# Performance work log

Measured on AMD Instinct MI355X. Metric: run time of the kernel, lower is better.

Reference implementation:

```python
import jax, jax.numpy as jnp
import numpy as np

D_MODEL = 1024
D_HEAD = 64
M_BITS = 32


def setup_inputs() -> dict:
    key = jax.random.key(0)
    ks = jax.random.split(key, 6)
    B, N, M = 2, 2048, 2048
    Q = jax.random.normal(ks[0], (B, N, D_MODEL), dtype=jnp.float32)
    K = jax.random.normal(ks[1], (B, M, D_MODEL), dtype=jnp.float32)
    V = jax.random.normal(ks[2], (B, M, D_MODEL), dtype=jnp.float32)
    s = 1.0 / np.sqrt(D_MODEL)
    Wq = jax.random.normal(ks[3], (D_MODEL, M_BITS), dtype=jnp.float32) * s
    Wk = jax.random.normal(ks[4], (D_MODEL, M_BITS), dtype=jnp.float32) * s
    Wv = jax.random.normal(ks[5], (D_MODEL, D_HEAD), dtype=jnp.float32) * s
    temperature = jnp.ones((1,), dtype=jnp.float32)
    return {"Q": Q, "K": K, "V": V, "Wq": Wq, "Wk": Wk, "Wv": Wv,
            "temperature": temperature}


def tropical_matmul(A, Bt):
    # A: [B, N, m], Bt: [B, M, m] (already transposed form of [B, m, M])
    # (A \odot B)_{ij} = min_k (A_ik + B_kj)
    return jnp.min(A[:, :, None, :] + Bt[:, None, :, :], axis=-1)  # [B, N, M]


def reference(Q, K, V, Wq, Wk, Wv, temperature):
    # REWA tropical encoders (continuous): linear projections to m_bits
    Qt = jnp.einsum('bnd,dm->bnm', Q, Wq)   # [B, N, m_bits]
    Kt = jnp.einsum('bsd,dm->bsm', K, Wk)   # [B, M, m_bits]
    Vp = jnp.einsum('bsd,dh->bsh', V, Wv)   # [B, M, d_head]
    # tropical (min-plus) scores, negated so shorter paths score higher
    scores = -tropical_matmul(Qt, Kt)       # [B, N, M]
    scores = scores / jax.nn.softplus(temperature[0])
    attn = jax.nn.softmax(scores, axis=-1)  # [B, N, M]
    out = jnp.einsum('bnm,bmh->bnh', attn, Vp)  # [B, N, d_head]
    return out, attn
```

## Files before the change

### kernel.cpp

```cpp
#include <hip/hip_runtime.h>
#include <math.h>

#define DM 1024
#define NB 2048
#define MBITS 32
#define DH 64

typedef __attribute__((ext_vector_type(4))) float floatx4;
typedef __attribute__((ext_vector_type(8))) short shortx8;

__device__ __forceinline__ unsigned short f32_to_bf16(float f) {
    union { float f; unsigned u; } v; v.f = f;
    unsigned r = v.u + 0x7FFF + ((v.u >> 16) & 1);
    return (unsigned short)(r >> 16);
}

__device__ __forceinline__ void split2(float x0, float x1, unsigned& hp, unsigned& lp) {
    union { float f; unsigned u; } a, b; a.f = x0; b.f = x1;
    unsigned h0 = a.u & 0xFFFF0000u, h1 = b.u & 0xFFFF0000u;
    union { unsigned u; float f; } hf0, hf1; hf0.u = h0; hf1.u = h1;
    union { float f; unsigned u; } c, d;
    c.f = x0 - hf0.f;
    d.f = x1 - hf1.f;
    hp = (h0 >> 16) | h1;
    lp = (c.u >> 16) | (d.u & 0xFFFF0000u);
}

__global__ __launch_bounds__(256) void wprep_kernel(
    const float* __restrict__ Wq, const float* __restrict__ Wk,
    const float* __restrict__ Wv, unsigned short* __restrict__ Wf)
{
    int wv = blockIdx.x * 4 + (threadIdx.x >> 6);
    int l  = threadIdx.x & 63;
    const float* W; int C, kc32, ct;
    if (wv < 64)       { W = Wq; C = 32; kc32 = wv >> 1;  ct = wv & 1; }
    else if (wv < 128) { W = Wk; C = 32; int z = wv - 64;  kc32 = z >> 1; ct = z & 1; }
    else               { W = Wv; C = 64; int z = wv - 128; kc32 = z >> 2; ct = z & 3; }
    int k0 = kc32 * 32 + (l >> 4) * 8;
    int c  = ct * 16 + (l & 15);
    float x[8];
    #pragma unroll
    for (int j = 0; j < 8; ++j) x[j] = W[(size_t)(k0 + j) * C + c];
    unsigned hp[4], lp[4];
    #pragma unroll
    for (int j2 = 0; j2 < 4; ++j2) split2(x[2 * j2], x[2 * j2 + 1], hp[j2], lp[j2]);
    uint4 hv; hv.x = hp[0]; hv.y = hp[1]; hv.z = hp[2]; hv.w = hp[3];
    uint4 lv; lv.x = lp[0]; lv.y = lp[1]; lv.z = lp[2]; lv.w = lp[3];
    *(uint4*)&Wf[(size_t)wv * 1024 + l * 8]       = hv;
    *(uint4*)&Wf[(size_t)wv * 1024 + 512 + l * 8] = lv;
}

__global__ __launch_bounds__(512) void proj_mfma2_kernel(
    const float* __restrict__ Q, const float* __restrict__ K, const float* __restrict__ V,
    const unsigned short* __restrict__ Wf,
    float* __restrict__ Qt, float* __restrict__ KtT, unsigned short* __restrict__ VpT)
{
    __shared__ float red[8][64][16];

    int gb = blockIdx.x;
    int job = gb >> 8, tile = gb & 255;
    int r0 = tile * 16;
    const float* X = (job == 0) ? Q : (job == 1) ? K : V;
    int ntct  = (job == 2) ? 4 : 2;
    int pbase = job << 6;
    int t = threadIdx.x, w = t >> 6, l = t & 63;
    int lrow = l & 15, lq = l >> 4;

    const float* xrow = &X[(size_t)(r0 + lrow) * DM + w * 128 + lq * 8];

    floatx4 acc[4];
    #pragma unroll
    for (int i = 0; i < 4; ++i) acc[i] = (floatx4){0.f, 0.f, 0.f, 0.f};

    #pragma unroll
    for (int s = 0; s < 4; ++s) {
        floatx4 g0 = *(const floatx4*)(xrow + s * 32);
        floatx4 g1 = *(const floatx4*)(xrow + s * 32 + 4);
        union { unsigned u[4]; shortx8 v; } ahi, alo;
        split2(g0.x, g0.y, ahi.u[0], alo.u[0]);
        split2(g0.z, g0.w, ahi.u[1], alo.u[1]);
        split2(g1.x, g1.y, ahi.u[2], alo.u[2]);
        split2(g1.z, g1.w, ahi.u[3], alo.u[3]);
        int kc32 = w * 4 + s;
        #pragma unroll
        for (int ct = 0; ct < 4; ++ct) {
            if (ct >= ntct) break;
            int p = pbase + kc32 * ntct + ct;
            const unsigned short* wp = &Wf[(size_t)p * 1024 + l * 8];
            shortx8 bhi = *(const shortx8*)wp;
            shortx8 blo = *(const shortx8*)(wp + 512);
            acc[ct] = __builtin_amdgcn_mfma_f32_16x16x32_bf16(ahi.v, bhi, acc[ct], 0, 0, 0);
            acc[ct] = __builtin_amdgcn_mfma_f32_16x16x32_bf16(ahi.v, blo, acc[ct], 0, 0, 0);
            acc[ct] = __builtin_amdgcn_mfma_f32_16x16x32_bf16(alo.v, bhi, acc[ct], 0, 0, 0);
        }
    }

    #pragma unroll
    for (int ct = 0; ct < 4; ++ct) {
        if (ct >= ntct) break;
        #pragma unroll
        for (int r = 0; r < 4; ++r) red[w][l][ct * 4 + r] = acc[ct][r];
    }
    __syncthreads();

    int r = w & 3, ct0 = w >> 2;
    int row = r0 + lq * 4 + r;
    if (job == 0) {
        float v = red[0][l][ct0 * 4 + r] + red[1][l][ct0 * 4 + r]
                + red[2][l][ct0 * 4 + r] + red[3][l][ct0 * 4 + r]
                + red[4][l][ct0 * 4 + r] + red[5][l][ct0 * 4 + r]
                + red[6][l][ct0 * 4 + r] + red[7][l][ct0 * 4 + r];
        Qt[(size_t)row * MBITS + ct0 * 16 + lrow] = v;
    } else if (job == 1) {
        int bb = row >> 11, j = row & 2047;
        float v = red[0][l][ct0 * 4 + r] + red[1][l][ct0 * 4 + r]
                + red[2][l][ct0 * 4 + r] + red[3][l][ct0 * 4 + r]
                + red[4][l][ct0 * 4 + r] + red[5][l][ct0 * 4 + r]
                + red[6][l][ct0 * 4 + r] + red[7][l][ct0 * 4 + r];
        KtT[(size_t)bb * (MBITS * NB) + (size_t)(ct0 * 16 + lrow) * NB + j] = v;
    } else {
        int bb = row >> 11, j = row & 2047;
        #pragma unroll
        for (int cti = 0; cti < 2; ++cti) {
            int ct = ct0 + 2 * cti;
            float v = red[0][l][ct * 4 + r] + red[1][l][ct * 4 + r]
                    + red[2][l][ct * 4 + r] + red[3][l][ct * 4 + r]
                    + red[4][l][ct * 4 + r] + red[5][l][ct * 4 + r]
                    + red[6][l][ct * 4 + r] + red[7][l][ct * 4 + r];
            VpT[(size_t)bb * (DH * NB) + (size_t)(ct * 16 + lrow) * NB + j] = f32_to_bf16(v);
        }
    }
}

__global__ __attribute__((amdgpu_waves_per_eu(4, 4))) __launch_bounds__(1024)
void fused_score_out_kernel(
    const float* __restrict__ Qt, const float* __restrict__ KtT,
    const unsigned short* __restrict__ VpT, const float* __restrict__ temp,
    float* __restrict__ outp, float* __restrict__ attn)
{
    __shared__ unsigned short Elds[16][2056];
    __shared__ float redsum2[16][2];

    const int b  = blockIdx.y;
    const int i0 = blockIdx.x * 16;
    const int t  = threadIdx.x;
    const int w  = t >> 6, l = t & 63;

    const float tv = temp[0];
    const float c2 = -(1.0f / log1pf(__expf(tv))) * 1.44269504088896340736f;

    {
        const int ip  = w & 7;
        const int jhb = (w >> 3) * 1024;
        const int p   = l >> 4;
        const int l16 = l & 15;

        const float* Qbase = &Qt[(size_t)(b * NB + i0 + ip * 2) * MBITS + p * 8];
        floatx4 qa0 = *(const floatx4*)(Qbase);
        floatx4 qa1 = *(const floatx4*)(Qbase + 4);
        floatx4 qb0 = *(const floatx4*)(Qbase + MBITS);
        floatx4 qb1 = *(const floatx4*)(Qbase + MBITS + 4);

        const float* Kp = &KtT[(size_t)b * (MBITS * NB) + (size_t)(p * 8) * NB];
        float sacc0 = 0.f, sacc1 = 0.f;

        #pragma unroll 1
        for (int s = 0; s < 8; ++s) {
            const int j0 = jhb + s * 128 + l16 * 8;
            float m0[8], m1[8];
            #pragma unroll
            for (int jj = 0; jj < 8; ++jj) { m0[jj] = 1e30f; m1[jj] = 1e30f; }

            #pragma unroll
            for (int kp = 0; kp < 8; ++kp) {
                const float* kr = Kp + (size_t)kp * NB + j0;
                floatx4 k0 = *(const floatx4*)kr;
                floatx4 k1 = *(const floatx4*)(kr + 4);
                float qa = (kp < 4) ? qa0[kp] : qa1[kp - 4];
                float qb = (kp < 4) ? qb0[kp] : qb1[kp - 4];
                float kv[8] = {k0.x, k0.y, k0.z, k0.w, k1.x, k1.y, k1.z, k1.w};
                #pragma unroll
                for (int jj = 0; jj < 8; ++jj) {
                    m0[jj] = fminf(m0[jj], qa + kv[jj]);
                    m1[jj] = fminf(m1[jj], qb + kv[jj]);
                }
            }
            #pragma unroll
            for (int jj = 0; jj < 8; ++jj) {
                m0[jj] = fminf(m0[jj], __shfl_xor(m0[jj], 16, 64));
                m0[jj] = fminf(m0[jj], __shfl_xor(m0[jj], 32, 64));
                m1[jj] = fminf(m1[jj], __shfl_xor(m1[jj], 16, 64));
                m1[jj] = fminf(m1[jj], __shfl_xor(m1[jj], 32, 64));
            }
            float e0[8], e1[8];
            #pragma unroll
            for (int jj = 0; jj < 8; ++jj) {
                e0[jj] = exp2f(c2 * m0[jj]);
                e1[jj] = exp2f(c2 * m1[jj]);
            }
            uint4 u0, u1;
            u0.x = (unsigned)f32_to_bf16(e0[0]) | ((unsigned)f32_to_bf16(e0[1]) << 16);
            u0.y = (unsigned)f32_to_bf16(e0[2]) | ((unsigned)f32_to_bf16(e0[3]) << 16);
            u0.z = (unsigned)f32_to_bf16(e0[4]) | ((unsigned)f32_to_bf16(e0[5]) << 16);
            u0.w = (unsigned)f32_to_bf16(e0[6]) | ((unsigned)f32_to_bf16(e0[7]) << 16);
            u1.x = (unsigned)f32_to_bf16(e1[0]) | ((unsigned)f32_to_bf16(e1[1]) << 16);
            u1.y = (unsigned)f32_to_bf16(e1[2]) | ((unsigned)f32_to_bf16(e1[3]) << 16);
            u1.z = (unsigned)f32_to_bf16(e1[4]) | ((unsigned)f32_to_bf16(e1[5]) << 16);
            u1.w = (unsigned)f32_to_bf16(e1[6]) | ((unsigned)f32_to_bf16(e1[7]) << 16);
            if (l < 16) {
                *(uint4*)&Elds[ip * 2][j0]     = u0;
                *(uint4*)&Elds[ip * 2 + 1][j0] = u1;
            }
            float s0 = ((e0[0] + e0[1]) + (e0[2] + e0[3])) + ((e0[4] + e0[5]) + (e0[6] + e0[7]));
            float s1 = ((e1[0] + e1[1]) + (e1[2] + e1[3])) + ((e1[4] + e1[5]) + (e1[6] + e1[7]));
            #pragma unroll
            for (int off = 1; off < 16; off <<= 1) {
                s0 += __shfl_xor(s0, off, 64);
                s1 += __shfl_xor(s1, off, 64);
            }
            sacc0 += s0; sacc1 += s1;
        }
        if (l == 0) { redsum2[w][0] = sacc0; redsum2[w][1] = sacc1; }
    }
    __syncthreads();

    const int mrow = l & 15, q4 = l >> 4;
    const int hh  = (w & 3) * 16 + mrow;
    const int kg  = w >> 2;
    floatx4 acc = {0.f, 0.f, 0.f, 0.f};
    const unsigned short* Vb = &VpT[(size_t)b * (DH * NB) + (size_t)hh * NB];

    #pragma unroll
    for (int jc2 = 0; jc2 < 8; ++jc2) {
        #pragma unroll
        for (int t2 = 0; t2 < 2; ++t2) {
            int ks = kg * 2 + t2;
            int joff = jc2 * 256 + ks * 32 + q4 * 8;
            shortx8 a  = *(const shortx8*)&Elds[mrow][joff];
            shortx8 bf = *(const shortx8*)&Vb[joff];
            acc = __builtin_amdgcn_mfma_f32_16x16x32_bf16(a, bf, acc, 0, 0, 0);
        }
    }

    {
        float iv = 1.0f / (redsum2[w >> 1][w & 1] + redsum2[8 + (w >> 1)][w & 1]);
        #pragma unroll
        for (int u = 0; u < 8; ++u) {
            int j = u * 256 + l * 4;
            uint2 pk = *(const uint2*)&Elds[w][j];
            union { unsigned u; float f; } x0, x1, x2, x3;
            x0.u = pk.x << 16; x1.u = pk.x & 0xFFFF0000u;
            x2.u = pk.y << 16; x3.u = pk.y & 0xFFFF0000u;
            floatx4 o;
            o.x = x0.f * iv; o.y = x1.f * iv; o.z = x2.f * iv; o.w = x3.f * iv;
            *(floatx4*)&attn[(size_t)(b * NB + i0 + w) * 2048 + j] = o;
        }
    }
    __syncthreads();

    float* redCf = (float*)&Elds[0][0];
    if (w >= 4) *(floatx4*)&redCf[(((w - 4) * 64) + l) * 4] = acc;
    __syncthreads();
    if (w < 4) {
        floatx4 v0 = *(const floatx4*)&redCf[((w * 64) + l) * 4];
        floatx4 v1 = *(const floatx4*)&redCf[(((w + 4) * 64) + l) * 4];
        floatx4 v2 = *(const floatx4*)&redCf[(((w + 8) * 64) + l) * 4];
        #pragma unroll
        for (int r = 0; r < 4; ++r) {
            int irow = q4 * 4 + r;
            float ivr = 1.0f / (redsum2[irow >> 1][irow & 1]
                              + redsum2[8 + (irow >> 1)][irow & 1]);
            float v = ((acc[r] + v0[r]) + (v1[r] + v2[r]));
            outp[(size_t)(b * NB + i0 + irow) * DH + w * 16 + mrow] = v * ivr;
        }
    }
}

extern "C" void kernel_launch(void* const* d_in, const int* in_sizes, int n_in,
                              void* d_out, int out_size, void* d_ws, size_t ws_size,
                              hipStream_t stream) {
    (void)in_sizes; (void)n_in; (void)out_size; (void)ws_size;
    const float* Q    = (const float*)d_in[0];
    const float* K    = (const float*)d_in[1];
    const float* V    = (const float*)d_in[2];
    const float* Wq   = (const float*)d_in[3];
    const float* Wk   = (const float*)d_in[4];
    const float* Wv   = (const float*)d_in[5];
    const float* temp = (const float*)d_in[6];

    float* outp = (float*)d_out;
    float* attn = outp + 2 * 2048 * 64;

    char* ws = (char*)d_ws;
    float*          Qt  = (float*)(ws);
    float*          KtT = (float*)(ws + 524288);
    unsigned short* Wf  = (unsigned short*)(ws + 1179648);
    unsigned short* VpT = (unsigned short*)(ws + 1703936);

    wprep_kernel<<<64, 256, 0, stream>>>(Wq, Wk, Wv, Wf);
    proj_mfma2_kernel<<<768, 512, 0, stream>>>(Q, K, V, Wf, Qt, KtT, VpT);
    fused_score_out_kernel<<<dim3(128, 2), 1024, 0, stream>>>(Qt, KtT, VpT, temp, outp, attn);
}
```

Baseline: 152.2 us.

## Retile tropical score loop: each lane owns 8 rows x 4 columns, full k-reduction

Reworks the min-plus score phase so each wave handles 8 query rows by 256 columns, with each lane computing all 32 k terms for 4 columns instead of splitting k across lane groups. This removes the cross-lane shuffle min-reduction and raises register reuse of loaded K values across 8 rows. Row sums are now stored per wave and row, and summed over 8 column chunks at normalization time. The cost is more Q loads per lane (broadcast reads), 32 accumulators per lane, and a full 64-lane sum reduction per row.

Result: faster. 145.6 us (-4.4%).

```diff
diff --git a/kernel.cpp b/kernel.cpp
--- a/kernel.cpp
+++ b/kernel.cpp
@@ -139,7 +139,7 @@
     float* __restrict__ outp, float* __restrict__ attn)
 {
     __shared__ unsigned short Elds[16][2056];
-    __shared__ float redsum2[16][2];
+    __shared__ float redsum[16][8];
 
     const int b  = blockIdx.y;
     const int i0 = blockIdx.x * 16;
@@ -150,77 +150,57 @@
     const float c2 = -(1.0f / log1pf(__expf(tv))) * 1.44269504088896340736f;
 
     {
-        const int ip  = w & 7;
-        const int jhb = (w >> 3) * 1024;
-        const int p   = l >> 4;
-        const int l16 = l & 15;
-
-        const float* Qbase = &Qt[(size_t)(b * NB + i0 + ip * 2) * MBITS + p * 8];
-        floatx4 qa0 = *(const floatx4*)(Qbase);
-        floatx4 qa1 = *(const floatx4*)(Qbase + 4);
-        floatx4 qb0 = *(const floatx4*)(Qbase + MBITS);
-        floatx4 qb1 = *(const floatx4*)(Qbase + MBITS + 4);
-
-        const float* Kp = &KtT[(size_t)b * (MBITS * NB) + (size_t)(p * 8) * NB];
-        float sacc0 = 0.f, sacc1 = 0.f;
+        const int rg = w & 1;
+        const int jc = w >> 1;
+        const int j0 = jc * 256 + l * 4;
+
+        const float* Qb = &Qt[(size_t)(b * NB + i0 + rg * 8) * MBITS];
+        const float* Kb = &KtT[(size_t)b * (MBITS * NB) + j0];
+
+        float m[8][4];
+        #pragma unroll
+        for (int r = 0; r < 8; ++r)
+            #pragma unroll
+            for (int jj = 0; jj < 4; ++jj) m[r][jj] = 1e30f;
 
         #pragma unroll 1
-        for (int s = 0; s < 8; ++s) {
-            const int j0 = jhb + s * 128 + l16 * 8;
-            float m0[8], m1[8];
-            #pragma unroll
-            for (int jj = 0; jj < 8; ++jj) { m0[jj] = 1e30f; m1[jj] = 1e30f; }
-
-            #pragma unroll
-            for (int kp = 0; kp < 8; ++kp) {
-                const float* kr = Kp + (size_t)kp * NB + j0;
-                floatx4 k0 = *(const floatx4*)kr;
-                floatx4 k1 = *(const floatx4*)(kr + 4);
-                float qa = (kp < 4) ? qa0[kp] : qa1[kp - 4];
-                float qb = (kp < 4) ? qb0[kp] : qb1[kp - 4];
-                float kv[8] = {k0.x, k0.y, k0.z, k0.w, k1.x, k1.y, k1.z, k1.w};
+        for (int kc = 0; kc < 8; ++kc) {
+            floatx4 kv[4];
+            #pragma unroll
+            for (int k2 = 0; k2 < 4; ++k2)
+                kv[k2] = *(const floatx4*)(Kb + (size_t)(kc * 4 + k2) * NB);
+            floatx4 qv[8];
+            #pragma unroll
+            for (int r = 0; r < 8; ++r)
+                qv[r] = *(const floatx4*)(Qb + r * MBITS + kc * 4);
+            #pragma unroll
+            for (int r = 0; r < 8; ++r) {
                 #pragma unroll
-                for (int jj = 0; jj < 8; ++jj) {
-                    m0[jj] = fminf(m0[jj], qa + kv[jj]);
-                    m1[jj] = fminf(m1[jj], qb + kv[jj]);
+                for (int k2 = 0; k2 < 4; ++k2) {
+                    float q = qv[r][k2];
+                    m[r][0] = fminf(m[r][0], q + kv[k2].x);
+                    m[r][1] = fminf(m[r][1], q + kv[k2].y);
+                    m[r][2] = fminf(m[r][2], q + kv[k2].z);
+                    m[r][3] = fminf(m[r][3], q + kv[k2].w);
                 }
             }
-            #pragma unroll
-            for (int jj = 0; jj < 8; ++jj) {
-                m0[jj] = fminf(m0[jj], __shfl_xor(m0[jj], 16, 64));
-                m0[jj] = fminf(m0[jj], __shfl_xor(m0[jj], 32, 64));
-                m1[jj] = fminf(m1[jj], __shfl_xor(m1[jj], 16, 64));
-                m1[jj] = fminf(m1[jj], __shfl_xor(m1[jj], 32, 64));
-            }
-            float e0[8], e1[8];
-            #pragma unroll
-            for (int jj = 0; jj < 8; ++jj) {
-                e0[jj] = exp2f(c2 * m0[jj]);
-                e1[jj] = exp2f(c2 * m1[jj]);
-            }
-            uint4 u0, u1;
-            u0.x = (unsigned)f32_to_bf16(e0[0]) | ((unsigned)f32_to_bf16(e0[1]) << 16);
-            u0.y = (unsigned)f32_to_bf16(e0[2]) | ((unsigned)f32_to_bf16(e0[3]) << 16);
-            u0.z = (unsigned)f32_to_bf16(e0[4]) | ((unsigned)f32_to_bf16(e0[5]) << 16);
-            u0.w = (unsigned)f32_to_bf16(e0[6]) | ((unsigned)f32_to_bf16(e0[7]) << 16);
-            u1.x = (unsigned)f32_to_bf16(e1[0]) | ((unsigned)f32_to_bf16(e1[1]) << 16);
-            u1.y = (unsigned)f32_to_bf16(e1[2]) | ((unsigned)f32_to_bf16(e1[3]) << 16);
-            u1.z = (unsigned)f32_to_bf16(e1[4]) | ((unsigned)f32_to_bf16(e1[5]) << 16);
-            u1.w = (unsigned)f32_to_bf16(e1[6]) | ((unsigned)f32_to_bf16(e1[7]) << 16);
-            if (l < 16) {
-                *(uint4*)&Elds[ip * 2][j0]     = u0;
-                *(uint4*)&Elds[ip * 2 + 1][j0] = u1;
-            }
-            float s0 = ((e0[0] + e0[1]) + (e0[2] + e0[3])) + ((e0[4] + e0[5]) + (e0[6] + e0[7]));
-            float s1 = ((e1[0] + e1[1]) + (e1[2] + e1[3])) + ((e1[4] + e1[5]) + (e1[6] + e1[7]));
-            #pragma unroll
-            for (int off = 1; off < 16; off <<= 1) {
-                s0 += __shfl_xor(s0, off, 64);
-                s1 += __shfl_xor(s1, off, 64);
-            }
-            sacc0 += s0; sacc1 += s1;
-        }
-        if (l == 0) { redsum2[w][0] = sacc0; redsum2[w][1] = sacc1; }
+        }
+
+        #pragma unroll
+        for (int r = 0; r < 8; ++r) {
+            float e0 = exp2f(c2 * m[r][0]);
+            float e1 = exp2f(c2 * m[r][1]);
+            float e2 = exp2f(c2 * m[r][2]);
+            float e3 = exp2f(c2 * m[r][3]);
+            uint2 pk;
+            pk.x = (unsigned)f32_to_bf16(e0) | ((unsigned)f32_to_bf16(e1) << 16);
+            pk.y = (unsigned)f32_to_bf16(e2) | ((unsigned)f32_to_bf16(e3) << 16);
+            *(uint2*)&Elds[rg * 8 + r][j0] = pk;
+            float s = (e0 + e1) + (e2 + e3);
+            #pragma unroll
+            for (int off = 1; off < 64; off <<= 1) s += __shfl_xor(s, off, 64);
+            if (l == 0) redsum[w][r] = s;
+        }
     }
     __syncthreads();
 
@@ -243,7 +223,10 @@
     }
 
     {
-        float iv = 1.0f / (redsum2[w >> 1][w & 1] + redsum2[8 + (w >> 1)][w & 1]);
+        float s = 0.f;
+        #pragma unroll
+        for (int g = 0; g < 8; ++g) s += redsum[(w >> 3) + 2 * g][w & 7];
+        float iv = 1.0f / s;
         #pragma unroll
         for (int u = 0; u < 8; ++u) {
             int j = u * 256 + l * 4;
@@ -268,8 +251,10 @@
         #pragma unroll
         for (int r = 0; r < 4; ++r) {
             int irow = q4 * 4 + r;
-            float ivr = 1.0f / (redsum2[irow >> 1][irow & 1]
-                              + redsum2[8 + (irow >> 1)][irow & 1]);
+            float sr = 0.f;
+            #pragma unroll
+            for (int g = 0; g < 8; ++g) sr += redsum[(irow >> 3) + 2 * g][irow & 7];
+            float ivr = 1.0f / sr;
             float v = ((acc[r] + v0[r]) + (v1[r] + v2[r]));
             outp[(size_t)(b * NB + i0 + irow) * DH + w * 16 + mrow] = v * ivr;
         }
```
